# Optimization experiments

Measured on AMD Instinct MI355X. Metric: run time of the kernel, lower is better.

## Reference

```python
import jax, jax.numpy as jnp
import numpy as np

QP_ITERS = 500          # projected-gradient iterations on the dual (converges for this tiny QP)
S_PEN = 1000.0          # slack penalty from the cvxpy objective
BN_EPS = 1e-5


def batchnorm(x, gamma, beta):
    # x: (B, N, C); BatchNorm1d training-mode stats over (batch, points)
    mu = x.mean(axis=(0, 1))
    var = x.var(axis=(0, 1))
    return (x - mu) * jax.lax.rsqrt(var + BN_EPS) * gamma + beta


def solve_qp(p, G, h):
    # min_z,s 0.5||z-p||^2 + 1000||s||^2  s.t. G z <= h + s, s >= 0
    # Dual (eliminating z = p - G^T lam, s = lam/(2*1000)):
    #   min_{lam>=0} 0.5 lam^T M lam - lam^T q,  M = G G^T + I/(2*S_PEN), q = G p - h
    nc = G.shape[1]
    M = jnp.einsum('bcv,bdv->bcd', G, G) + jnp.eye(nc, dtype=G.dtype) / (2.0 * S_PEN)
    q = jnp.einsum('bcv,bv->bc', G, p) - h
    # safe step size: 1/trace(M) <= 1/lambda_max(M)
    alpha = jax.lax.stop_gradient(1.0 / jnp.trace(M, axis1=1, axis2=2))[:, None]

    def step(lam, _):
        grad = jnp.einsum('bcd,bd->bc', M, lam) - q
        return jnp.maximum(lam - alpha * grad, 0.0), None

    lam0 = jnp.zeros_like(q)
    lam, _ = jax.lax.scan(step, lam0, None, length=QP_ITERS)
    z = p - jnp.einsum('bcv,bc->bv', G, lam)
    return z


def setup_inputs() -> dict:
    key = jax.random.key(0)
    ks = jax.random.split(key, 16)
    B, N, NC = 64, 8192, 12

    def w(k, shape, s):
        return (jax.random.normal(k, shape) * s).astype(jnp.float32)

    bc2 = jnp.concatenate([w(ks[10], (NC * 3,), 0.02), jnp.full((NC,), 0.02, jnp.float32)])
    return {
        'pcd': jax.random.normal(ks[0], (B, N, 3), dtype=jnp.float32),
        # MiniPointNet (1x1 convs as matmuls) + batchnorm affine params
        'W1': w(ks[1], (64, 3), 0.4), 'b1': jnp.zeros(64), 'g1': jnp.ones(64), 'be1': jnp.zeros(64),
        'W2': w(ks[2], (128, 64), 0.1), 'b2': jnp.zeros(128), 'g2': jnp.ones(128), 'be2': jnp.zeros(128),
        'W3': w(ks[3], (256, 128), 0.07), 'b3': jnp.zeros(256), 'g3': jnp.ones(256), 'be3': jnp.zeros(256),
        'Wfc': w(ks[4], (128, 256), 0.05), 'bfc': jnp.zeros(128),
        # constraint_net: 128 -> 128 -> 48
        'Wc1': w(ks[5], (128, 128), 0.08), 'bc1': jnp.zeros(128),
        'Wc2': w(ks[6], (NC * 4, 128), 0.08), 'bc2': bc2,
        # p_net: 128 -> 64 -> 7 (last layer ~N(0, 0.001), zero bias)
        'Wp1': w(ks[7], (64, 128), 0.08), 'bp1': jnp.zeros(64),
        'Wp2': w(ks[8], (7, 64), 0.001), 'bp2': jnp.zeros(7),
    }


def reference(pcd, W1, b1, g1, be1, W2, b2, g2, be2, W3, b3, g3, be3,
              Wfc, bfc, Wc1, bc1, Wc2, bc2, Wp1, bp1, Wp2, bp2):
    B = pcd.shape[0]
    NC = bc2.shape[0] // 4
    # MiniPointNet: pointwise MLP + global max pool
    x = jax.nn.relu(batchnorm(pcd @ W1.T + b1, g1, be1))     # (B,N,64)
    x = jax.nn.relu(batchnorm(x @ W2.T + b2, g2, be2))       # (B,N,128)
    x = jax.nn.relu(batchnorm(x @ W3.T + b3, g3, be3))       # (B,N,256)
    feats = x.max(axis=1) @ Wfc.T + bfc                       # (B,128)

    raw_p = jax.nn.relu(feats @ Wp1.T + bp1) @ Wp2.T + bp2    # (B,7)
    p_pred = jnp.concatenate([
        jnp.tanh(raw_p[:, :3]) * 0.1,
        jnp.tanh(raw_p[:, 3:6]) * 1.57,
        jnp.tanh(raw_p[:, 6:7]) * 0.05], axis=1)

    out_cons = (jax.nn.relu(feats @ Wc1.T + bc1) @ Wc2.T + bc2).reshape(B, NC, 4)
    normals = out_cons[:, :, :3]
    # F.normalize(p=2, dim=2): clamp norm at 1e-12
    normals = normals / jnp.clip(jnp.linalg.norm(normals, axis=2, keepdims=True), 1e-12)
    h = jax.nn.softplus(out_cons[:, :, 3]) + 0.005            # (B,NC)
    G = jnp.concatenate([normals, jnp.zeros((B, NC, 4), normals.dtype)], axis=2)  # (B,NC,7)

    delta_norm = solve_qp(p_pred, G, h)                       # (B,7)
    return delta_norm, normals, h, p_pred
```

## Files before the change

kernel.cpp:

```cpp
#include <hip/hip_runtime.h>
#include <hip/hip_bf16.h>

#define NPTS 524288
#define NBATCH 64

typedef __attribute__((ext_vector_type(8))) short bf16x8;
typedef __attribute__((ext_vector_type(4))) float f32x4;
typedef const float* __restrict__ fp;

__device__ __forceinline__ __hip_bfloat16 f2b(float v) { return __float2bfloat16(v); }
__device__ __forceinline__ unsigned bfbits(float v) {
    union { __hip_bfloat16 h; unsigned short s; } u; u.h = f2b(v); return (unsigned)u.s;
}
__device__ __forceinline__ unsigned pk2(float a, float b) {
    return bfbits(a) | (bfbits(b) << 16);
}

__device__ __forceinline__ unsigned fkey(float f) {
    unsigned u = __float_as_uint(f);
    return u ^ ((u & 0x80000000u) ? 0xFFFFFFFFu : 0x80000000u);
}
__device__ __forceinline__ float funkey(unsigned k) {
    unsigned u = (k & 0x80000000u) ? (k ^ 0x80000000u) : ~k;
    return __uint_as_float(u);
}

union U8 { bf16x8 v; __hip_bfloat16 e[8]; unsigned u[4]; };

static __device__ __forceinline__ f32x4 mfma16(bf16x8 a, bf16x8 b, f32x4 c) {
    return __builtin_amdgcn_mfma_f32_16x16x32_bf16(a, b, c, 0, 0, 0);
}

__global__ void k_prep(fp W2, fp W3, __hip_bfloat16* __restrict__ W2b,
                       __hip_bfloat16* __restrict__ W3b)
{
    int i = blockIdx.x * blockDim.x + threadIdx.x;
    if (i < 8192) W2b[i] = f2b(W2[i]);
    const int j = i - 8192;
    if (j >= 0 && j < 32768) W3b[j] = f2b(W3[j]);
}

__launch_bounds__(256)
__global__ void k_moments(fp pcd, float* __restrict__ mom)
{
    float s[9];
#pragma unroll
    for (int i = 0; i < 9; ++i) s[i] = 0.f;
    const int stride = gridDim.x * blockDim.x;
    for (int p = blockIdx.x * blockDim.x + threadIdx.x; p < NPTS; p += stride) {
        const float x = pcd[3*p+0], y = pcd[3*p+1], z = pcd[3*p+2];
        s[0] += x; s[1] += y; s[2] += z;
        s[3] = fmaf(x, x, s[3]); s[4] = fmaf(x, y, s[4]); s[5] = fmaf(x, z, s[5]);
        s[6] = fmaf(y, y, s[6]); s[7] = fmaf(y, z, s[7]); s[8] = fmaf(z, z, s[8]);
    }
#pragma unroll
    for (int off = 1; off < 64; off <<= 1) {
#pragma unroll
        for (int i = 0; i < 9; ++i) s[i] += __shfl_xor(s[i], off);
    }
    __shared__ float red[4][9];
    const int lane = threadIdx.x & 63, wv = threadIdx.x >> 6;
    if (lane == 0) {
#pragma unroll
        for (int i = 0; i < 9; ++i) red[wv][i] = s[i];
    }
    __syncthreads();
    if (threadIdx.x < 9) {
        const int i = threadIdx.x;
        atomicAdd(&mom[i], red[0][i] + red[1][i] + red[2][i] + red[3][i]);
    }
}

__global__ void k_fin1(const float* __restrict__ mom, fp W1, fp b1, fp g1, fp be1,
                       unsigned* __restrict__ W1p)
{
    const int c = threadIdx.x;
    const float inv = 1.f / (float)NPTS;
    const float m0 = mom[0]*inv, m1 = mom[1]*inv, m2 = mom[2]*inv;
    const float c00 = mom[3]*inv - m0*m0, c01 = mom[4]*inv - m0*m1, c02 = mom[5]*inv - m0*m2;
    const float c11 = mom[6]*inv - m1*m1, c12 = mom[7]*inv - m1*m2, c22 = mom[8]*inv - m2*m2;
    const float w0 = W1[c*3+0], w1 = W1[c*3+1], w2 = W1[c*3+2];
    const float mu = w0*m0 + w1*m1 + w2*m2 + b1[c];
    float var = w0*w0*c00 + w1*w1*c11 + w2*w2*c22 + 2.f*(w0*w1*c01 + w0*w2*c02 + w1*w2*c12);
    var = fmaxf(var, 0.f);
    const float sc = g1[c] * rsqrtf(var + 1e-5f);
    const float sh = be1[c] - mu*sc;
    W1p[c*2+0] = pk2(w0*sc, w1*sc);
    W1p[c*2+1] = pk2(w2*sc, b1[c]*sc + sh);
}

#define L1_AND_REDIST(a2f)                                                      \
    {                                                                           \
        unsigned u1s[4][2];                                                     \
        _Pragma("unroll")                                                       \
        for (int nt = 0; nt < 4; ++nt) {                                        \
            f32x4 c1 = mfma16(wb1[nt], a1.v, (f32x4){0.f,0.f,0.f,0.f});         \
            u1s[nt][0] = pk2(fmaxf(c1[0],0.f), fmaxf(c1[1],0.f));               \
            u1s[nt][1] = pk2(fmaxf(c1[2],0.f), fmaxf(c1[3],0.f));               \
        }                                                                       \
        const int srcBase = m + ((q & 1) ? 32 : 0);                             \
        _Pragma("unroll")                                                       \
        for (int ks = 0; ks < 2; ++ks) {                                        \
            _Pragma("unroll")                                                   \
            for (int t2 = 0; t2 < 4; ++t2) {                                    \
                const int src = srcBase + 16*(t2>>1);                           \
                const unsigned rlo = (unsigned)__shfl((int)u1s[2*ks  ][t2&1], src); \
                const unsigned rhi = (unsigned)__shfl((int)u1s[2*ks+1][t2&1], src); \
                a2f[ks].u[t2] = (q >= 2) ? rhi : rlo;                           \
            }                                                                   \
        }                                                                       \
    }

__launch_bounds__(256, 3)
__global__ void k_pass1(fp pcd, const unsigned* __restrict__ W1p,
                        const __hip_bfloat16* __restrict__ W2b,
                        float* __restrict__ st2s, float* __restrict__ st2q)
{
    __shared__ float red[1024];
    const int tid = threadIdx.x, wv = tid >> 6, lane = tid & 63;
    const int m = lane & 15, q = lane >> 4;
    const int batch = blockIdx.x >> 5, sub = blockIdx.x & 31;

    bf16x8 wb1[4];
#pragma unroll
    for (int nt = 0; nt < 4; ++nt) {
        U8 w; w.u[0] = w.u[1] = w.u[2] = w.u[3] = 0;
        if (q == 0) { w.u[0] = W1p[(nt*16+m)*2]; w.u[1] = W1p[(nt*16+m)*2+1]; }
        wb1[nt] = w.v;
    }
    bf16x8 wb2[8][2];
#pragma unroll
    for (int nt = 0; nt < 8; ++nt) {
#pragma unroll
        for (int kk = 0; kk < 2; ++kk)
            wb2[nt][kk] = *(const bf16x8*)(W2b + (nt*16+m)*64 + kk*32 + q*8);
    }

    float s_acc[8], q_acc[8];
#pragma unroll
    for (int nt = 0; nt < 8; ++nt) { s_acc[nt] = 0.f; q_acc[nt] = 0.f; }

    for (int it = 0; it < 4; ++it) {
        const int p0 = batch*8192 + sub*256 + it*64 + wv*16;
        const float* pp = pcd + (size_t)(p0 + m) * 3;
        const float cx = pp[0], cy = pp[1], cz = pp[2];
        U8 a1; a1.u[0] = a1.u[1] = a1.u[2] = a1.u[3] = 0;
        if (q == 0) { a1.u[0] = pk2(cx, cy); a1.u[1] = pk2(cz, 1.f); }

        U8 a2f[2];
        L1_AND_REDIST(a2f)

#pragma unroll
        for (int nt = 0; nt < 8; ++nt) {
            f32x4 c = mfma16(a2f[0].v, wb2[nt][0], (f32x4){0.f,0.f,0.f,0.f});
            c = mfma16(a2f[1].v, wb2[nt][1], c);
            s_acc[nt] += (c[0] + c[1]) + (c[2] + c[3]);
            q_acc[nt] = fmaf(c[0],c[0], fmaf(c[1],c[1], fmaf(c[2],c[2], fmaf(c[3],c[3], q_acc[nt]))));
        }
    }
#pragma unroll
    for (int nt = 0; nt < 8; ++nt) {
        s_acc[nt] += __shfl_xor(s_acc[nt], 16); q_acc[nt] += __shfl_xor(q_acc[nt], 16);
        s_acc[nt] += __shfl_xor(s_acc[nt], 32); q_acc[nt] += __shfl_xor(q_acc[nt], 32);
    }
    if (q == 0) {
#pragma unroll
        for (int nt = 0; nt < 8; ++nt) {
            red[wv*128 + nt*16 + m] = s_acc[nt];
            red[512 + wv*128 + nt*16 + m] = q_acc[nt];
        }
    }
    __syncthreads();
    if (tid < 128) {
        float s = 0.f, ss = 0.f;
#pragma unroll
        for (int w4 = 0; w4 < 4; ++w4) { s += red[w4*128 + tid]; ss += red[512 + w4*128 + tid]; }
        const int slot = blockIdx.x & 63;
        atomicAdd(&st2s[slot*128 + tid], s);
        atomicAdd(&st2q[slot*128 + tid], ss);
    }
}

__global__ void k_fin2(const float* __restrict__ sum, const float* __restrict__ sq,
                       fp g, fp be, float* __restrict__ sOut, float* __restrict__ tOut)
{
    const int ch = threadIdx.x;
    float s = 0.f, ss = 0.f;
    for (int slot = 0; slot < 64; ++slot) { s += sum[slot*128 + ch]; ss += sq[slot*128 + ch]; }
    const float inv = 1.f / (float)NPTS;
    const float mu = s * inv;
    const float var = fmaxf(ss * inv - mu*mu, 0.f);
    const float sc = g[ch] * rsqrtf(var + 1e-5f);
    sOut[ch] = sc;
    tOut[ch] = be[ch] - mu*sc;
}

__launch_bounds__(256, 2)
__global__ void k_pass2(fp pcd, const unsigned* __restrict__ W1p,
                        const __hip_bfloat16* __restrict__ W2b,
                        const float* __restrict__ s2, const float* __restrict__ t2,
                        const __hip_bfloat16* __restrict__ W3b,
                        float* __restrict__ st3s, float* __restrict__ st3q,
                        unsigned* __restrict__ maxk, unsigned* __restrict__ mink)
{
    __shared__ alignas(16) __hip_bfloat16 x2s[2][64*136];
    const int tid = threadIdx.x, wv = tid >> 6, lane = tid & 63;
    const int m = lane & 15, q = lane >> 4;
    const int batch = blockIdx.x >> 5, sub = blockIdx.x & 31;

    bf16x8 wb1[4];
#pragma unroll
    for (int nt = 0; nt < 4; ++nt) {
        U8 w; w.u[0] = w.u[1] = w.u[2] = w.u[3] = 0;
        if (q == 0) { w.u[0] = W1p[(nt*16+m)*2]; w.u[1] = W1p[(nt*16+m)*2+1]; }
        wb1[nt] = w.v;
    }
    bf16x8 wb2[8][2];
#pragma unroll
    for (int nt = 0; nt < 8; ++nt) {
#pragma unroll
        for (int kk = 0; kk < 2; ++kk)
            wb2[nt][kk] = *(const bf16x8*)(W2b + (nt*16+m)*64 + kk*32 + q*8);
    }
    float s2v[8], t2v[8];
#pragma unroll
    for (int nt = 0; nt < 8; ++nt) { s2v[nt] = s2[nt*16+m]; t2v[nt] = t2[nt*16+m]; }

    bf16x8 wb3[4][4];
#pragma unroll
    for (int nt = 0; nt < 4; ++nt) {
        const int ch3 = wv*64 + nt*16 + m;
#pragma unroll
        for (int ks = 0; ks < 4; ++ks)
            wb3[nt][ks] = *(const bf16x8*)(W3b + ch3*128 + ks*32 + q*8);
    }

    float s3[4], q3[4], mx3[4], mn3[4];
#pragma unroll
    for (int nt = 0; nt < 4; ++nt) { s3[nt]=0.f; q3[nt]=0.f; mx3[nt]=-3.4e38f; mn3[nt]=3.4e38f; }

    for (int it = 0; it < 4; ++it) {
        __hip_bfloat16* xb = x2s[it & 1];
        const int p0 = batch*8192 + sub*256 + it*64 + wv*16;
        const float* pp = pcd + (size_t)(p0 + m) * 3;
        const float cx = pp[0], cy = pp[1], cz = pp[2];
        U8 a1; a1.u[0] = a1.u[1] = a1.u[2] = a1.u[3] = 0;
        if (q == 0) { a1.u[0] = pk2(cx, cy); a1.u[1] = pk2(cz, 1.f); }

        U8 a2f[2];
        L1_AND_REDIST(a2f)

#pragma unroll
        for (int nt = 0; nt < 8; ++nt) {
            f32x4 c = mfma16(a2f[0].v, wb2[nt][0], (f32x4){0.f,0.f,0.f,0.f});
            c = mfma16(a2f[1].v, wb2[nt][1], c);
#pragma unroll
            for (int r = 0; r < 4; ++r) {
                const float v = fmaxf(fmaf(c[r], s2v[nt], t2v[nt]), 0.f);
                const unsigned own = bfbits(v);
                const unsigned oth = (unsigned)__shfl_xor((int)own, 1);
                if ((m & 1) == 0) {
                    const int row = wv*16 + q*4 + r;
                    *(unsigned*)&xb[row*136 + nt*16 + m] = own | (oth << 16);
                }
            }
        }
        __syncthreads();
#pragma unroll
        for (int ms = 0; ms < 4; ++ms) {
            const int rowM = (ms*16 + m) * 136;
            bf16x8 a3[4];
#pragma unroll
            for (int ks = 0; ks < 4; ++ks)
                a3[ks] = *(const bf16x8*)&xb[rowM + ks*32 + q*8];
#pragma unroll
            for (int nt = 0; nt < 4; ++nt) {
                f32x4 c = mfma16(a3[0], wb3[nt][0], (f32x4){0.f,0.f,0.f,0.f});
                c = mfma16(a3[1], wb3[nt][1], c);
                c = mfma16(a3[2], wb3[nt][2], c);
                c = mfma16(a3[3], wb3[nt][3], c);
                s3[nt] += (c[0] + c[1]) + (c[2] + c[3]);
                q3[nt] = fmaf(c[0],c[0], fmaf(c[1],c[1], fmaf(c[2],c[2], fmaf(c[3],c[3], q3[nt]))));
                mx3[nt] = fmaxf(fmaxf(c[0], c[1]), fmaxf(fmaxf(c[2], c[3]), mx3[nt]));
                mn3[nt] = fminf(fminf(c[0], c[1]), fminf(fminf(c[2], c[3]), mn3[nt]));
            }
        }
    }
#pragma unroll
    for (int nt = 0; nt < 4; ++nt) {
        s3[nt] += __shfl_xor(s3[nt], 16);  q3[nt] += __shfl_xor(q3[nt], 16);
        mx3[nt] = fmaxf(mx3[nt], __shfl_xor(mx3[nt], 16));
        mn3[nt] = fminf(mn3[nt], __shfl_xor(mn3[nt], 16));
        s3[nt] += __shfl_xor(s3[nt], 32);  q3[nt] += __shfl_xor(q3[nt], 32);
        mx3[nt] = fmaxf(mx3[nt], __shfl_xor(mx3[nt], 32));
        mn3[nt] = fminf(mn3[nt], __shfl_xor(mn3[nt], 32));
    }
    if (q == 0) {
        const int slot = blockIdx.x & 63;
#pragma unroll
        for (int nt = 0; nt < 4; ++nt) {
            const int ch3 = wv*64 + nt*16 + m;
            atomicAdd(&st3s[slot*256 + ch3], s3[nt]);
            atomicAdd(&st3q[slot*256 + ch3], q3[nt]);
            atomicMax(&maxk[batch*256 + ch3], fkey(mx3[nt]));
            atomicMin(&mink[batch*256 + ch3], fkey(mn3[nt]));
        }
    }
}

__launch_bounds__(128)
__global__ void k_head(const float* __restrict__ st3s, const float* __restrict__ st3q,
                       fp g3, fp be3,
                       const unsigned* __restrict__ maxk, const unsigned* __restrict__ mink,
                       fp Wfc, fp bfc, fp Wc1, fp bc1, fp Wc2, fp bc2,
                       fp Wp1, fp bp1, fp Wp2, fp bp2,
                       float* __restrict__ out)
{
    __shared__ float pf[256], ft[128], hcs[128], hps[64], ocs[48], nrm[36], hS[12], pp[8];
    const int bb = blockIdx.x, tid = threadIdx.x;
#pragma unroll
    for (int h = 0; h < 2; ++h) {
        const int ch = tid + h*128;
        float s = 0.f, ss = 0.f;
        for (int slot = 0; slot < 64; ++slot) { s += st3s[slot*256 + ch]; ss += st3q[slot*256 + ch]; }
        const float inv = 1.f / (float)NPTS;
        const float mu = s * inv;
        const float var = fmaxf(ss * inv - mu*mu, 0.f);
        const float sc = g3[ch] * rsqrtf(var + 1e-5f);
        const float sh = be3[ch] - mu*sc;
        const float pick = (sc >= 0.f) ? funkey(maxk[bb*256 + ch]) : funkey(mink[bb*256 + ch]);
        pf[ch] = fmaxf(fmaf(pick, sc, sh), 0.f);
    }
    __syncthreads();
    {
        float a = bfc[tid];
        const float* wr = Wfc + tid*256;
        for (int k = 0; k < 256; ++k) a = fmaf(pf[k], wr[k], a);
        ft[tid] = a;
    }
    __syncthreads();
    {
        float a = bc1[tid];
        const float* wr = Wc1 + tid*128;
        for (int k = 0; k < 128; ++k) a = fmaf(ft[k], wr[k], a);
        hcs[tid] = fmaxf(a, 0.f);
    }
    if (tid < 64) {
        float a = bp1[tid];
        const float* wr = Wp1 + tid*128;
        for (int k = 0; k < 128; ++k) a = fmaf(ft[k], wr[k], a);
        hps[tid] = fmaxf(a, 0.f);
    }
    __syncthreads();
    if (tid < 48) {
        float a = bc2[tid];
        const float* wr = Wc2 + tid*128;
        for (int k = 0; k < 128; ++k) a = fmaf(hcs[k], wr[k], a);
        ocs[tid] = a;
    }
    if (tid < 7) {
        float a = bp2[tid];
        const float* wr = Wp2 + tid*64;
        for (int k = 0; k < 64; ++k) a = fmaf(hps[k], wr[k], a);
        const float sc = (tid < 3) ? 0.1f : ((tid < 6) ? 1.57f : 0.05f);
        pp[tid] = tanhf(a) * sc;
    }
    __syncthreads();
    if (tid < 12) {
        float nx = ocs[tid*4+0], ny = ocs[tid*4+1], nz = ocs[tid*4+2];
        const float nn = fmaxf(sqrtf(nx*nx + ny*ny + nz*nz), 1e-12f);
        const float inv = 1.f / nn;
        nx *= inv; ny *= inv; nz *= inv;
        nrm[tid*3+0] = nx; nrm[tid*3+1] = ny; nrm[tid*3+2] = nz;
        const float xx = ocs[tid*4+3];
        hS[tid] = ((xx > 20.f) ? xx : log1pf(expf(xx))) + 0.005f;
    }
    __syncthreads();

    const int lane = tid & 63;
    const int c = (lane < 12) ? lane : 11;
    const float n0 = nrm[c*3+0], n1 = nrm[c*3+1], n2 = nrm[c*3+2];
    float Mrow[12];
    float trace = 0.f;
#pragma unroll
    for (int d = 0; d < 12; ++d) {
        const float d0 = nrm[d*3+0], d1 = nrm[d*3+1], d2 = nrm[d*3+2];
        Mrow[d] = n0*d0 + n1*d1 + n2*d2 + ((d == lane) ? 5e-4f : 0.f);
        trace += d0*d0 + d1*d1 + d2*d2;
    }
    const float alpha = 1.f / (trace + 12.f*5e-4f);
    const float qc = n0*pp[0] + n1*pp[1] + n2*pp[2] - hS[c];
    float lam = 0.f;
    for (int it = 0; it < 500; ++it) {
        const float l0 = __shfl(lam, 0),  l1 = __shfl(lam, 1),  l2 = __shfl(lam, 2);
        const float l3 = __shfl(lam, 3),  l4 = __shfl(lam, 4),  l5 = __shfl(lam, 5);
        const float l6 = __shfl(lam, 6),  l7 = __shfl(lam, 7),  l8 = __shfl(lam, 8);
        const float l9 = __shfl(lam, 9),  l10 = __shfl(lam, 10), l11 = __shfl(lam, 11);
        const float g0 = fmaf(Mrow[0], l0, fmaf(Mrow[3], l3, fmaf(Mrow[6], l6, Mrow[9]*l9)));
        const float g1 = fmaf(Mrow[1], l1, fmaf(Mrow[4], l4, fmaf(Mrow[7], l7, Mrow[10]*l10)));
        const float g2 = fmaf(Mrow[2], l2, fmaf(Mrow[5], l5, fmaf(Mrow[8], l8, Mrow[11]*l11)));
        lam = fmaxf(fmaf(-alpha, g0 + g1 + g2 - qc, lam), 0.f);
    }
    float v0 = (lane < 12) ? n0*lam : 0.f;
    float v1 = (lane < 12) ? n1*lam : 0.f;
    float v2 = (lane < 12) ? n2*lam : 0.f;
#pragma unroll
    for (int off = 1; off <= 8; off <<= 1) {
        v0 += __shfl_xor(v0, off);
        v1 += __shfl_xor(v1, off);
        v2 += __shfl_xor(v2, off);
    }
    if (tid < 7) {
        float z;
        if (tid == 0) z = pp[0] - v0;
        else if (tid == 1) z = pp[1] - v1;
        else if (tid == 2) z = pp[2] - v2;
        else z = pp[tid];
        out[bb*7 + tid] = z;
    }
    if (tid < 36) out[448 + bb*36 + tid] = nrm[tid];
    if (tid < 12) out[2752 + bb*12 + tid] = hS[tid];
    if (tid < 7)  out[3520 + bb*7 + tid] = pp[tid];
}

extern "C" void kernel_launch(void* const* d_in, const int* in_sizes, int n_in,
                              void* d_out, int out_size, void* d_ws, size_t ws_size,
                              hipStream_t stream) {
    fp pcd = (fp)d_in[0];
    fp W1 = (fp)d_in[1],  fp_b1 = (fp)d_in[2],  g1 = (fp)d_in[3],  be1 = (fp)d_in[4];
    fp W2 = (fp)d_in[5],  g2 = (fp)d_in[7],  be2 = (fp)d_in[8];
    fp W3 = (fp)d_in[9],  g3 = (fp)d_in[11], be3 = (fp)d_in[12];
    fp Wfc = (fp)d_in[13], bfc = (fp)d_in[14];
    fp Wc1 = (fp)d_in[15], bc1 = (fp)d_in[16];
    fp Wc2 = (fp)d_in[17], bc2 = (fp)d_in[18];
    fp Wp1 = (fp)d_in[19], bp1 = (fp)d_in[20];
    fp Wp2 = (fp)d_in[21], bp2 = (fp)d_in[22];

    float* ws = (float*)d_ws;
    float* mom  = ws + 0;
    float* s2   = ws + 144;
    float* t2   = ws + 272;
    float* st2s = ws + 400;
    float* st2q = ws + 8592;
    float* st3s = ws + 16784;
    float* st3q = ws + 33168;
    unsigned* maxk = (unsigned*)(ws + 49552);
    unsigned* mink = (unsigned*)(ws + 65936);
    __hip_bfloat16* W2b = (__hip_bfloat16*)(ws + 82320);
    __hip_bfloat16* W3b = (__hip_bfloat16*)(ws + 86416);
    unsigned* W1p = (unsigned*)(ws + 102800);
    if (ws_size < (size_t)102928 * 4) return;

    hipMemsetAsync(d_ws, 0, (size_t)65936 * 4, stream);
    hipMemsetAsync((void*)mink, 0xFF, (size_t)16384 * 4, stream);

    k_prep<<<160, 256, 0, stream>>>(W2, W3, W2b, W3b);
    k_moments<<<1024, 256, 0, stream>>>(pcd, mom);
    k_fin1<<<1, 64, 0, stream>>>(mom, W1, fp_b1, g1, be1, W1p);
    k_pass1<<<2048, 256, 0, stream>>>(pcd, W1p, W2b, st2s, st2q);
    k_fin2<<<1, 128, 0, stream>>>(st2s, st2q, g2, be2, s2, t2);
    k_pass2<<<2048, 256, 0, stream>>>(pcd, W1p, W2b, s2, t2, W3b,
                                      st3s, st3q, maxk, mink);
    k_head<<<64, 128, 0, stream>>>(st3s, st3q, g3, be3, maxk, mink,
                                   Wfc, bfc, Wc1, bc1, Wc2, bc2,
                                   Wp1, bp1, Wp2, bp2, (float*)d_out);
}
```

Before: 319.1 us.

## Compute layer 1 with scalar FMAs and batch layer 3 over full tile

```diff
diff --git a/kernel.cpp b/kernel.cpp
--- a/kernel.cpp
+++ b/kernel.cpp
@@ -15,6 +15,8 @@
 __device__ __forceinline__ unsigned pk2(float a, float b) {
     return bfbits(a) | (bfbits(b) << 16);
 }
+__device__ __forceinline__ float lo2f(unsigned u) { return __uint_as_float(u << 16); }
+__device__ __forceinline__ float hi2f(unsigned u) { return __uint_as_float(u & 0xffff0000u); }
 
 __device__ __forceinline__ unsigned fkey(float f) {
     unsigned u = __float_as_uint(f);
@@ -89,26 +91,29 @@
     W1p[c*2+1] = pk2(w2*sc, b1[c]*sc + sh);
 }
 
-#define L1_AND_REDIST(a2f)                                                      \
+#define L1_DIRECT(a2f, px, py, pz)                                              \
     {                                                                           \
-        unsigned u1s[4][2];                                                     \
+        float y[16];                                                            \
         _Pragma("unroll")                                                       \
-        for (int nt = 0; nt < 4; ++nt) {                                        \
-            f32x4 c1 = mfma16(wb1[nt], a1.v, (f32x4){0.f,0.f,0.f,0.f});         \
-            u1s[nt][0] = pk2(fmaxf(c1[0],0.f), fmaxf(c1[1],0.f));               \
-            u1s[nt][1] = pk2(fmaxf(c1[2],0.f), fmaxf(c1[3],0.f));               \
+        for (int t = 0; t < 16; ++t) {                                          \
+            float v = fmaf(px, lo2f(wA[t]), hi2f(wB[t]));                       \
+            v = fmaf(py, hi2f(wA[t]), v);                                       \
+            v = fmaf(pz, lo2f(wB[t]), v);                                       \
+            y[t] = fmaxf(v, 0.f);                                               \
         }                                                                       \
-        const int srcBase = m + ((q & 1) ? 32 : 0);                             \
         _Pragma("unroll")                                                       \
-        for (int ks = 0; ks < 2; ++ks) {                                        \
+        for (int ks = 0; ks < 2; ++ks)                                          \
             _Pragma("unroll")                                                   \
-            for (int t2 = 0; t2 < 4; ++t2) {                                    \
-                const int src = srcBase + 16*(t2>>1);                           \
-                const unsigned rlo = (unsigned)__shfl((int)u1s[2*ks  ][t2&1], src); \
-                const unsigned rhi = (unsigned)__shfl((int)u1s[2*ks+1][t2&1], src); \
-                a2f[ks].u[t2] = (q >= 2) ? rhi : rlo;                           \
-            }                                                                   \
-        }                                                                       \
+            for (int t2 = 0; t2 < 4; ++t2)                                      \
+                a2f[ks].u[t2] = pk2(y[ks*8 + 2*t2], y[ks*8 + 2*t2 + 1]);        \
+    }
+
+#define LOAD_W1()                                                               \
+    unsigned wA[16], wB[16];                                                    \
+    _Pragma("unroll")                                                           \
+    for (int t = 0; t < 16; ++t) {                                              \
+        const int ch = (t >> 3)*32 + q*8 + (t & 7);                             \
+        wA[t] = W1p[ch*2]; wB[t] = W1p[ch*2+1];                                 \
     }
 
 __launch_bounds__(256, 3)
@@ -121,13 +126,7 @@
     const int m = lane & 15, q = lane >> 4;
     const int batch = blockIdx.x >> 5, sub = blockIdx.x & 31;
 
-    bf16x8 wb1[4];
-#pragma unroll
-    for (int nt = 0; nt < 4; ++nt) {
-        U8 w; w.u[0] = w.u[1] = w.u[2] = w.u[3] = 0;
-        if (q == 0) { w.u[0] = W1p[(nt*16+m)*2]; w.u[1] = W1p[(nt*16+m)*2+1]; }
-        wb1[nt] = w.v;
-    }
+    LOAD_W1()
     bf16x8 wb2[8][2];
 #pragma unroll
     for (int nt = 0; nt < 8; ++nt) {
@@ -140,16 +139,13 @@
 #pragma unroll
     for (int nt = 0; nt < 8; ++nt) { s_acc[nt] = 0.f; q_acc[nt] = 0.f; }
 
+#pragma unroll
     for (int it = 0; it < 4; ++it) {
         const int p0 = batch*8192 + sub*256 + it*64 + wv*16;
         const float* pp = pcd + (size_t)(p0 + m) * 3;
-        const float cx = pp[0], cy = pp[1], cz = pp[2];
-        U8 a1; a1.u[0] = a1.u[1] = a1.u[2] = a1.u[3] = 0;
-        if (q == 0) { a1.u[0] = pk2(cx, cy); a1.u[1] = pk2(cz, 1.f); }
-
+        const float px = pp[0], py = pp[1], pz = pp[2];
         U8 a2f[2];
-        L1_AND_REDIST(a2f)
-
+        L1_DIRECT(a2f, px, py, pz)
 #pragma unroll
         for (int nt = 0; nt < 8; ++nt) {
             f32x4 c = mfma16(a2f[0].v, wb2[nt][0], (f32x4){0.f,0.f,0.f,0.f});
@@ -203,18 +199,12 @@
                         float* __restrict__ st3s, float* __restrict__ st3q,
                         unsigned* __restrict__ maxk, unsigned* __restrict__ mink)
 {
-    __shared__ alignas(16) __hip_bfloat16 x2s[2][64*136];
+    __shared__ alignas(16) __hip_bfloat16 x2s[256*136];
     const int tid = threadIdx.x, wv = tid >> 6, lane = tid & 63;
     const int m = lane & 15, q = lane >> 4;
     const int batch = blockIdx.x >> 5, sub = blockIdx.x & 31;
 
-    bf16x8 wb1[4];
-#pragma unroll
-    for (int nt = 0; nt < 4; ++nt) {
-        U8 w; w.u[0] = w.u[1] = w.u[2] = w.u[3] = 0;
-        if (q == 0) { w.u[0] = W1p[(nt*16+m)*2]; w.u[1] = W1p[(nt*16+m)*2+1]; }
-        wb1[nt] = w.v;
-    }
+    LOAD_W1()
     bf16x8 wb2[8][2];
 #pragma unroll
     for (int nt = 0; nt < 8; ++nt) {
@@ -235,21 +225,13 @@
             wb3[nt][ks] = *(const bf16x8*)(W3b + ch3*128 + ks*32 + q*8);
     }
 
-    float s3[4], q3[4], mx3[4], mn3[4];
-#pragma unroll
-    for (int nt = 0; nt < 4; ++nt) { s3[nt]=0.f; q3[nt]=0.f; mx3[nt]=-3.4e38f; mn3[nt]=3.4e38f; }
-
+#pragma unroll
     for (int it = 0; it < 4; ++it) {
-        __hip_bfloat16* xb = x2s[it & 1];
         const int p0 = batch*8192 + sub*256 + it*64 + wv*16;
         const float* pp = pcd + (size_t)(p0 + m) * 3;
-        const float cx = pp[0], cy = pp[1], cz = pp[2];
-        U8 a1; a1.u[0] = a1.u[1] = a1.u[2] = a1.u[3] = 0;
-        if (q == 0) { a1.u[0] = pk2(cx, cy); a1.u[1] = pk2(cz, 1.f); }
-
+        const float px = pp[0], py = pp[1], pz = pp[2];
         U8 a2f[2];
-        L1_AND_REDIST(a2f)
-
+        L1_DIRECT(a2f, px, py, pz)
 #pragma unroll
         for (int nt = 0; nt < 8; ++nt) {
             f32x4 c = mfma16(a2f[0].v, wb2[nt][0], (f32x4){0.f,0.f,0.f,0.f});
@@ -260,30 +242,34 @@
                 const unsigned own = bfbits(v);
                 const unsigned oth = (unsigned)__shfl_xor((int)own, 1);
                 if ((m & 1) == 0) {
-                    const int row = wv*16 + q*4 + r;
-                    *(unsigned*)&xb[row*136 + nt*16 + m] = own | (oth << 16);
+                    const int row = it*64 + wv*16 + q*4 + r;
+                    *(unsigned*)&x2s[row*136 + nt*16 + m] = own | (oth << 16);
                 }
             }
         }
-        __syncthreads();
-#pragma unroll
-        for (int ms = 0; ms < 4; ++ms) {
-            const int rowM = (ms*16 + m) * 136;
-            bf16x8 a3[4];
-#pragma unroll
-            for (int ks = 0; ks < 4; ++ks)
-                a3[ks] = *(const bf16x8*)&xb[rowM + ks*32 + q*8];
-#pragma unroll
-            for (int nt = 0; nt < 4; ++nt) {
-                f32x4 c = mfma16(a3[0], wb3[nt][0], (f32x4){0.f,0.f,0.f,0.f});
-                c = mfma16(a3[1], wb3[nt][1], c);
-                c = mfma16(a3[2], wb3[nt][2], c);
-                c = mfma16(a3[3], wb3[nt][3], c);
-                s3[nt] += (c[0] + c[1]) + (c[2] + c[3]);
-                q3[nt] = fmaf(c[0],c[0], fmaf(c[1],c[1], fmaf(c[2],c[2], fmaf(c[3],c[3], q3[nt]))));
-                mx3[nt] = fmaxf(fmaxf(c[0], c[1]), fmaxf(fmaxf(c[2], c[3]), mx3[nt]));
-                mn3[nt] = fminf(fminf(c[0], c[1]), fminf(fminf(c[2], c[3]), mn3[nt]));
-            }
+    }
+    __syncthreads();
+
+    float s3[4], q3[4], mx3[4], mn3[4];
+#pragma unroll
+    for (int nt = 0; nt < 4; ++nt) { s3[nt]=0.f; q3[nt]=0.f; mx3[nt]=-3.4e38f; mn3[nt]=3.4e38f; }
+
+    for (int ms = 0; ms < 16; ++ms) {
+        const int rowM = (ms*16 + m) * 136;
+        bf16x8 a3[4];
+#pragma unroll
+        for (int ks = 0; ks < 4; ++ks)
+            a3[ks] = *(const bf16x8*)&x2s[rowM + ks*32 + q*8];
+#pragma unroll
+        for (int nt = 0; nt < 4; ++nt) {
+            f32x4 c = mfma16(a3[0], wb3[nt][0], (f32x4){0.f,0.f,0.f,0.f});
+            c = mfma16(a3[1], wb3[nt][1], c);
+            c = mfma16(a3[2], wb3[nt][2], c);
+            c = mfma16(a3[3], wb3[nt][3], c);
+            s3[nt] += (c[0] + c[1]) + (c[2] + c[3]);
+            q3[nt] = fmaf(c[0],c[0], fmaf(c[1],c[1], fmaf(c[2],c[2], fmaf(c[3],c[3], q3[nt]))));
+            mx3[nt] = fmaxf(fmaxf(c[0], c[1]), fmaxf(fmaxf(c[2], c[3]), mx3[nt]));
+            mn3[nt] = fminf(fminf(c[0], c[1]), fminf(fminf(c[2], c[3]), mn3[nt]));
         }
     }
 #pragma unroll
@@ -427,7 +413,7 @@
                               void* d_out, int out_size, void* d_ws, size_t ws_size,
                               hipStream_t stream) {
     fp pcd = (fp)d_in[0];
-    fp W1 = (fp)d_in[1],  fp_b1 = (fp)d_in[2],  g1 = (fp)d_in[3],  be1 = (fp)d_in[4];
+    fp W1 = (fp)d_in[1],  b1 = (fp)d_in[2],  g1 = (fp)d_in[3],  be1 = (fp)d_in[4];
     fp W2 = (fp)d_in[5],  g2 = (fp)d_in[7],  be2 = (fp)d_in[8];
     fp W3 = (fp)d_in[9],  g3 = (fp)d_in[11], be3 = (fp)d_in[12];
     fp Wfc = (fp)d_in[13], bfc = (fp)d_in[14];
@@ -456,7 +442,7 @@
 
     k_prep<<<160, 256, 0, stream>>>(W2, W3, W2b, W3b);
     k_moments<<<1024, 256, 0, stream>>>(pcd, mom);
-    k_fin1<<<1, 64, 0, stream>>>(mom, W1, fp_b1, g1, be1, W1p);
+    k_fin1<<<1, 64, 0, stream>>>(mom, W1, b1, g1, be1, W1p);
     k_pass1<<<2048, 256, 0, stream>>>(pcd, W1p, W2b, st2s, st2q);
     k_fin2<<<1, 128, 0, stream>>>(st2s, st2q, g2, be2, s2, t2);
     k_pass2<<<2048, 256, 0, stream>>>(pcd, W1p, W2b, s2, t2, W3b,
```

Result: faster. 293.8 us (-7.9%).
